# Optimization experiments

Hardware: AMD Instinct MI355X
Metric: run time of the kernel (lower is better)

The kernel has to match this reference:

```python
import jax, jax.numpy as jnp
import numpy as np

EPS_NORM = 1e-8   # matches torch F.normalize default-ish eps used in cosine_dist
CLAMP_MIN = 1e-12
CLAMP_MAX = 1e12

def setup_inputs() -> dict:
    key = jax.random.key(0)
    k1, k2, k3 = jax.random.split(key, 3)
    N, D, C = 262144, 256, 64
    ref_emb = jax.random.normal(k1, (N, D), dtype=jnp.float32)
    ref_label = jax.random.randint(k2, (N,), 0, C)
    centers = jax.random.normal(k3, (C, D), dtype=jnp.float32)
    return {"ref_emb": ref_emb, "ref_label": ref_label, "centers": centers}

def reference(ref_emb, ref_label, centers):
    # center[i] = centers[ref_label[i]]  -> [N, D] gather
    center = centers[ref_label]
    # diag of pairwise cosine-distance matrix == row-wise cosine distance
    # cos_dist_i = 1 - <x_i, c_i> / (||x_i|| * ||c_i||)
    dot = jnp.sum(ref_emb * center, axis=-1)                     # [N]
    nx = jnp.sqrt(jnp.sum(ref_emb * ref_emb, axis=-1))           # [N]
    nc = jnp.sqrt(jnp.sum(center * center, axis=-1))             # [N]
    cos_sim = dot / jnp.maximum(nx * nc, EPS_NORM)
    cos_diag = 1.0 - cos_sim
    return jnp.mean(jnp.clip(cos_diag, CLAMP_MIN, CLAMP_MAX), axis=-1)
```

## Files before the change

### kernel.cpp

```cpp
#include <hip/hip_runtime.h>
#include <math.h>

constexpr int N = 262144;
constexpr int D = 256;
constexpr int C = 64;
constexpr float EPS_NORM  = 1e-8f;
constexpr float CLAMP_MIN = 1e-12f;
constexpr float CLAMP_MAX = 1e12f;

__global__ __launch_bounds__(64) void center_norm_kernel(
        const float* __restrict__ centers, float* __restrict__ cnorm) {
    const int c = blockIdx.x;
    const int lane = threadIdx.x;
    float4 v = reinterpret_cast<const float4*>(centers + c * D)[lane];
    float s = v.x * v.x + v.y * v.y + v.z * v.z + v.w * v.w;
    #pragma unroll
    for (int off = 32; off >= 1; off >>= 1)
        s += __shfl_xor(s, off, 64);
    if (lane == 0) cnorm[c] = sqrtf(s);
}

__global__ __launch_bounds__(256) void inner_cos_kernel(
        const float* __restrict__ emb,
        const int*   __restrict__ label,
        const float* __restrict__ centers,
        const float* __restrict__ cnorm,
        float* __restrict__ out) {
    const int lane  = threadIdx.x & 63;
    const int wave  = threadIdx.x >> 6;
    const int gwave = (blockIdx.x << 2) | wave;
    const int nwave = gridDim.x << 2;

    float lsum = 0.0f;
    for (int row = gwave; row < N; row += nwave) {
        const int lab = label[row];
        const float4 x = reinterpret_cast<const float4*>(emb + (size_t)row * D)[lane];
        const float4 c = reinterpret_cast<const float4*>(centers + lab * D)[lane];

        float dot = x.x * c.x + x.y * c.y + x.z * c.z + x.w * c.w;
        float nx2 = x.x * x.x + x.y * x.y + x.z * x.z + x.w * x.w;

        #pragma unroll
        for (int off = 32; off >= 1; off >>= 1) {
            dot += __shfl_xor(dot, off, 64);
            nx2 += __shfl_xor(nx2, off, 64);
        }
        const float denom = fmaxf(sqrtf(nx2) * cnorm[lab], EPS_NORM);
        float cd = 1.0f - dot / denom;
        cd = fminf(fmaxf(cd, CLAMP_MIN), CLAMP_MAX);
        lsum += cd;
    }

    __shared__ float ssum[4];
    if (lane == 0) ssum[wave] = lsum;
    __syncthreads();
    if (threadIdx.x == 0) {
        const float s = (ssum[0] + ssum[1]) + (ssum[2] + ssum[3]);
        atomicAdd(out, s * (1.0f / (float)N));
    }
}

extern "C" void kernel_launch(void* const* d_in, const int* in_sizes, int n_in,
                              void* d_out, int out_size, void* d_ws, size_t ws_size,
                              hipStream_t stream) {
    const float* emb     = (const float*)d_in[0];
    const int*   label   = (const int*)d_in[1];
    const float* centers = (const float*)d_in[2];
    float* out   = (float*)d_out;
    float* cnorm = (float*)d_ws;

    hipMemsetAsync(d_out, 0, sizeof(float), stream);

    center_norm_kernel<<<C, 64, 0, stream>>>(centers, cnorm);

    inner_cos_kernel<<<2048, 256, 0, stream>>>(emb, label, centers, cnorm, out);
}
```

Before: 371.9 us.

## Process four rows per wave with 16-lane groups and deterministic two-stage reduction

Each wave now splits into four 16-lane groups, and each group handles one row with four float4 loads per lane. This raises memory-level parallelism and shortens the cross-lane shuffle reduction. The global atomicAdd and memset are replaced by per-block partial sums written to workspace plus a single-block finalize kernel. This adds one kernel launch but makes the final reduction deterministic.

```diff
diff --git a/kernel.cpp b/kernel.cpp
--- a/kernel.cpp
+++ b/kernel.cpp
@@ -7,6 +7,8 @@
 constexpr float EPS_NORM  = 1e-8f;
 constexpr float CLAMP_MIN = 1e-12f;
 constexpr float CLAMP_MAX = 1e12f;
+
+constexpr int BLOCKS = 2048;
 
 __global__ __launch_bounds__(64) void center_norm_kernel(
         const float* __restrict__ centers, float* __restrict__ cnorm) {
@@ -25,23 +27,34 @@
         const int*   __restrict__ label,
         const float* __restrict__ centers,
         const float* __restrict__ cnorm,
-        float* __restrict__ out) {
-    const int lane  = threadIdx.x & 63;
-    const int wave  = threadIdx.x >> 6;
-    const int gwave = (blockIdx.x << 2) | wave;
-    const int nwave = gridDim.x << 2;
+        float* __restrict__ partials) {
+    const int lane = threadIdx.x & 63;
+    const int wave = threadIdx.x >> 6;
+    const int sub  = lane & 15;
+    const int quad = lane >> 4;
+    const int gwave   = (blockIdx.x << 2) | wave;
+    const int ngroups = N >> 2;
+    const int nwave   = BLOCKS << 2;
 
     float lsum = 0.0f;
-    for (int row = gwave; row < N; row += nwave) {
+    for (int g = gwave; g < ngroups; g += nwave) {
+        const int row = (g << 2) | quad;
         const int lab = label[row];
-        const float4 x = reinterpret_cast<const float4*>(emb + (size_t)row * D)[lane];
-        const float4 c = reinterpret_cast<const float4*>(centers + lab * D)[lane];
+        const float4* xrow = reinterpret_cast<const float4*>(emb + (size_t)row * D);
+        const float4* crow = reinterpret_cast<const float4*>(centers + (size_t)lab * D);
 
-        float dot = x.x * c.x + x.y * c.y + x.z * c.z + x.w * c.w;
-        float nx2 = x.x * x.x + x.y * x.y + x.z * x.z + x.w * x.w;
-
+        float dot = 0.0f, nx2 = 0.0f;
         #pragma unroll
-        for (int off = 32; off >= 1; off >>= 1) {
+        for (int j = 0; j < 4; ++j) {
+            const float4 x = xrow[(j << 4) + sub];
+            const float4 c = crow[(j << 4) + sub];
+            dot = fmaf(x.x, c.x, dot); dot = fmaf(x.y, c.y, dot);
+            dot = fmaf(x.z, c.z, dot); dot = fmaf(x.w, c.w, dot);
+            nx2 = fmaf(x.x, x.x, nx2); nx2 = fmaf(x.y, x.y, nx2);
+            nx2 = fmaf(x.z, x.z, nx2); nx2 = fmaf(x.w, x.w, nx2);
+        }
+        #pragma unroll
+        for (int off = 8; off >= 1; off >>= 1) {
             dot += __shfl_xor(dot, off, 64);
             nx2 += __shfl_xor(nx2, off, 64);
         }
@@ -51,13 +64,30 @@
         lsum += cd;
     }
 
+    lsum += __shfl_xor(lsum, 16, 64);
+    lsum += __shfl_xor(lsum, 32, 64);
+
     __shared__ float ssum[4];
     if (lane == 0) ssum[wave] = lsum;
     __syncthreads();
-    if (threadIdx.x == 0) {
-        const float s = (ssum[0] + ssum[1]) + (ssum[2] + ssum[3]);
-        atomicAdd(out, s * (1.0f / (float)N));
-    }
+    if (threadIdx.x == 0)
+        partials[blockIdx.x] = (ssum[0] + ssum[1]) + (ssum[2] + ssum[3]);
+}
+
+__global__ __launch_bounds__(256) void finalize_kernel(
+        const float* __restrict__ partials, float* __restrict__ out) {
+    float s = 0.0f;
+    #pragma unroll
+    for (int i = 0; i < BLOCKS / 256; ++i)
+        s += partials[threadIdx.x + (i << 8)];
+    #pragma unroll
+    for (int off = 32; off >= 1; off >>= 1)
+        s += __shfl_xor(s, off, 64);
+    __shared__ float ss[4];
+    if ((threadIdx.x & 63) == 0) ss[threadIdx.x >> 6] = s;
+    __syncthreads();
+    if (threadIdx.x == 0)
+        out[0] = ((ss[0] + ss[1]) + (ss[2] + ss[3])) * (1.0f / (float)N);
 }
 
 extern "C" void kernel_launch(void* const* d_in, const int* in_sizes, int n_in,
@@ -66,12 +96,11 @@
     const float* emb     = (const float*)d_in[0];
     const int*   label   = (const int*)d_in[1];
     const float* centers = (const float*)d_in[2];
-    float* out   = (float*)d_out;
-    float* cnorm = (float*)d_ws;
-
-    hipMemsetAsync(d_out, 0, sizeof(float), stream);
+    float* out      = (float*)d_out;
+    float* cnorm    = (float*)d_ws;
+    float* partials = (float*)d_ws + 64;
 
     center_norm_kernel<<<C, 64, 0, stream>>>(centers, cnorm);
-
-    inner_cos_kernel<<<2048, 256, 0, stream>>>(emb, label, centers, cnorm, out);
+    inner_cos_kernel<<<BLOCKS, 256, 0, stream>>>(emb, label, centers, cnorm, partials);
+    finalize_kernel<<<1, 256, 0, stream>>>(partials, out);
 }
```

Result: faster. 358.3 us (-3.7%).
